# Kernel tuning notes

Hardware: AMD Instinct MI355X
Metric: run time of the kernel (lower is better)

## Reference

```python
import jax, jax.numpy as jnp
import numpy as np
from jax import lax

B, R, F = 100, 15, 4096       # batch, regions, feature dim
V, E, D, A, T = 10000, 1024, 1024, 512, 500  # vocab, embed, decoder, attention, topic
LIN = 1024                    # autoencoder linear output width
NT = 5                        # sentences per paragraph
L = 52                        # max caption length


def setup_inputs() -> dict:
    key = jax.random.key(0)
    ks = jax.random.split(key, 16)
    g = lambda i, shp, s: jax.random.normal(ks[i], shp, jnp.float32) * s
    return {
        "image_features": g(0, (B, R, F), 1.0),
        "encoded_captions": jax.random.randint(ks[1], (B, NT, L), 0, V),
        "caption_lengths": jax.random.randint(ks[2], (B, NT), 1, L),
        # autoencoder
        "W_lt": g(3, (LIN, F), 0.02), "b_lt": jnp.zeros((LIN,), jnp.float32),
        "conv_w": g(4, (6, 1, 15, 26), 0.05), "conv_b": jnp.zeros((6,), jnp.float32),
        # attention MLP (weight_norm linears == plain linears mathematically)
        "W_feat": g(5, (A, F), 0.02), "b_feat": jnp.zeros((A,), jnp.float32),
        "W_dec": g(6, (A, D), 0.02), "b_dec": jnp.zeros((A,), jnp.float32),
        "W_top": g(7, (A, T), 0.02), "b_top": jnp.zeros((A,), jnp.float32),
        "W_full": g(8, (1, A), 0.02), "b_full": jnp.zeros((1,), jnp.float32),
        # embedding + LSTM cells + output heads
        "emb": g(9, (V, E), 0.1),
        "W_ih1": g(10, (4 * D, E + F + D), 0.01), "W_hh1": g(11, (4 * D, D), 0.01),
        "b_ih1": jnp.zeros((4 * D,), jnp.float32), "b_hh1": jnp.zeros((4 * D,), jnp.float32),
        "W_ih2": g(12, (4 * D, F + D), 0.01), "W_hh2": g(13, (4 * D, D), 0.01),
        "b_ih2": jnp.zeros((4 * D,), jnp.float32), "b_hh2": jnp.zeros((4 * D,), jnp.float32),
        "W_fc1": g(14, (V, D), 0.02), "b_fc1": jnp.zeros((V,), jnp.float32),
        "W_fc": g(15, (V, D), 0.02), "b_fc": jnp.zeros((V,), jnp.float32),
    }


def _lstm_cell(x, h, c, W_ih, W_hh, b_ih, b_hh):
    gates = x @ W_ih.T + b_ih + h @ W_hh.T + b_hh
    i, f, g_, o = jnp.split(gates, 4, axis=-1)
    c = jax.nn.sigmoid(f) * c + jax.nn.sigmoid(i) * jnp.tanh(g_)
    h = jax.nn.sigmoid(o) * jnp.tanh(c)
    return h, c


def reference(image_features, encoded_captions, caption_lengths, W_lt, b_lt,
              conv_w, conv_b, W_feat, b_feat, W_dec, b_dec, W_top, b_top,
              W_full, b_full, emb, W_ih1, W_hh1, b_ih1, b_hh1,
              W_ih2, W_hh2, b_ih2, b_hh2, W_fc1, b_fc1, W_fc, b_fc):
    def per_sample(img, caps, lens):
        # img (R,F), caps (NT,L) int, lens (NT,) int
        img_mean = img.mean(0)  # (F,)
        # autoencoder: linear 4096->1024, conv2d(1->6, k=(15,26), stride 2)
        x = (img @ W_lt.T + b_lt)[None, None]  # (1,1,R,LIN)
        conv = lax.conv_general_dilated(x, conv_w, (2, 2), "VALID",
                                        dimension_numbers=("NCHW", "OIHW", "NCHW"))
        topics = conv[0, :, 0, :] + conv_b[:, None]  # (6, T=500)
        att1 = img @ W_feat.T + b_feat               # (R,A), precomputed once
        # last word of each sentence: caps[t, lens[t]-1]
        last_words = jnp.take_along_axis(caps, (lens - 1)[:, None], axis=1)[:, 0]  # (NT,)
        last_embs = emb[last_words]                  # (NT,E)

        def step(carry, tup):
            h1, c1, h2, c2 = carry
            topic_t, emb_t = tup
            # top-down attention LSTM: cat([h2, img_mean, word_emb])
            x1 = jnp.concatenate([h2, img_mean, emb_t])
            h1, c1 = _lstm_cell(x1, h1, c1, W_ih1, W_hh1, b_ih1, b_hh1)
            # attention over R regions (dropout is identity in eval)
            att = jax.nn.relu(att1 + (h1 @ W_dec.T + b_dec) + (topic_t @ W_top.T + b_top))
            scores = att @ W_full[0] + b_full[0]     # (R,)
            alpha = jax.nn.softmax(scores)
            awe = alpha @ img                        # (F,)
            preds1 = h1 @ W_fc1.T + b_fc1            # (V,)
            h2, c2 = _lstm_cell(jnp.concatenate([awe, h1]), h2, c2,
                                W_ih2, W_hh2, b_ih2, b_hh2)
            preds = h2 @ W_fc.T + b_fc               # (V,)
            return (h1, c1, h2, c2), (preds, preds1)

        z = jnp.zeros((D,), img.dtype)
        _, (preds, preds1) = lax.scan(step, (z, z, z, z), (topics[:NT], last_embs))
        return preds, preds1                          # (NT,V) each

    preds, preds1 = jax.vmap(per_sample)(image_features, encoded_captions, caption_lengths)
    return preds, preds1, encoded_captions, caption_lengths - 1
```

## Files before the change

kernel.cpp:

```cpp
#include <hip/hip_runtime.h>

typedef __attribute__((ext_vector_type(8))) short short8;
typedef __attribute__((ext_vector_type(4))) short short4v;
typedef __attribute__((ext_vector_type(4))) float f32x4;

__device__ __forceinline__ unsigned short f2bf(float f) {
  unsigned int u = __float_as_uint(f);
  u += 0x7fffu + ((u >> 16) & 1u);
  return (unsigned short)(u >> 16);
}
__device__ __forceinline__ float bf2f(unsigned short u) {
  return __uint_as_float(((unsigned int)u) << 16);
}
__device__ __forceinline__ float sigm(float x) { return 1.f / (1.f + expf(-x)); }

template<int NKC>
__global__ __launch_bounds__(256) void gemm_v5(
    const unsigned short* __restrict__ X, int ldx,
    const unsigned short* __restrict__ W, int ldw, int N,
    unsigned short* __restrict__ C, long long slotStride)
{
  __shared__ short8 lds[3584];
  const int tid = threadIdx.x;
  const int lane = tid & 63, wv = tid >> 6;
// ... 60 lines not shown
  const int nrow = (ncol < N) ? ncol : (N - 1);
  const long long k0 = (long long)blockIdx.z * (NKC * 256);
  C += (long long)blockIdx.z * slotStride;

  const float* wp = W + (size_t)nrow * ldw + kg + k0;
  const unsigned short* xb = X + (size_t)(mbase + l16) * ldx + kg + k0;
  const size_t xrow = (size_t)16 * ldx;

  f32x4 acc[7];
#pragma unroll
  for (int i = 0; i < 7; ++i) acc[i] = (f32x4){0.f, 0.f, 0.f, 0.f};

  for (int kc = 0; kc < NKC; ++kc) {
    if (kc) __syncthreads();
    float4 wa[8], wb[8];
#pragma unroll
    for (int ks = 0; ks < 8; ++ks) {
      wa[ks] = *(const float4*)(wp + kc * 256 + ks * 32);
      wb[ks] = *(const float4*)(wp + kc * 256 + ks * 32 + 4);
    }
    short8 xst[14];
#pragma unroll
    for (int i = 0; i < 14; ++i) {
      const int f = wv + i * 4, mt = f >> 3, ks = f & 7;
      xst[i] = *(const short8*)(xb + (size_t)mt * xrow + kc * 256 + ks * 32);
    }
#pragma unroll
    for (int i = 0; i < 14; ++i) lds[(wv + i * 4) * 64 + lane] = xst[i];
    __syncthreads();
#pragma unroll
    for (int ks = 0; ks < 8; ++ks) {
      short8 w;
      w[0] = (short)f2bf(wa[ks].x); w[1] = (short)f2bf(wa[ks].y);
      w[2] = (short)f2bf(wa[ks].z); w[3] = (short)f2bf(wa[ks].w);
      w[4] = (short)f2bf(wb[ks].x); w[5] = (short)f2bf(wb[ks].y);
      w[6] = (short)f2bf(wb[ks].z); w[7] = (short)f2bf(wb[ks].w);
#pragma unroll
      for (int mt = 0; mt < 7; ++mt) {
        short8 a = lds[(mt * 8 + ks) * 64 + lane];
        acc[mt] = __builtin_amdgcn_mfma_f32_16x16x32_bf16(a, w, acc[mt], 0, 0, 0);
      }
    }
  }
  if (ncol < N) {
    const int r0 = (lane >> 4) * 4;
#pragma unroll
    for (int mt = 0; mt < 7; ++mt)
#pragma unroll
      for (int r = 0; r < 4; ++r)
        C[(size_t)(mbase + mt * 16 + r0 + r) * N + ncol] = f2bf(acc[mt][r]);
  }
}

__global__ __launch_bounds__(256) void k_pack_all(
    const float* __restrict__ Wih1, const float* __restrict__ Whh1,
    const float* __restrict__ Wih2, const float* __restrict__ Whh2,
    const float* __restrict__ Wfc1, const float* __restrict__ Wdec,
    const float* __restrict__ Wfc,  const float* __restrict__ Wlt,
    const float* __restrict__ Wft,  const float* __restrict__ Wtop,
    unsigned short* __restrict__ Wg1, unsigned short* __restrict__ Wg2,
    unsigned short* __restrict__ Wcat, unsigned short* __restrict__ Wfcb,
    unsigned short* __restrict__ Wltb, unsigned short* __restrict__ Wftb,
    unsigned short* __restrict__ Wtopb)
{
  int i = blockIdx.x * 256 + threadIdx.x;
  float4 v; unsigned short* dst; long long di;
  if (i < 2097152) {
    int row = i >> 9, c4 = i & 511;
    const float* s = (c4 < 256) ? Wih1 + (size_t)row * 6144 + c4 * 4
                                : Whh1 + (size_t)row * 1024 + (c4 - 256) * 4;
    v = *(const float4*)s; dst = Wg1; di = i;
  } else if (i < 8388608) {
    int j = i - 2097152; int row = j / 1536, c4 = j - row * 1536;
    const float* s = (c4 < 1280) ? Wih2 + (size_t)row * 5120 + c4 * 4
                                 : Whh2 + (size_t)row * 1024 + (c4 - 1280) * 4;
    v = *(const float4*)s; dst = Wg2; di = j;
  } else if (i < 11079680) {
    int j = i - 8388608; int row = j >> 8, c4 = j & 255;
    const float* s = (row < 10000) ? Wfc1 + (size_t)row * 1024 + c4 * 4
                                   : Wdec + (size_t)(row - 10000) * 1024 + c4 * 4;
    v = *(const float4*)s; dst = Wcat; di = j;
  } else if (i < 13639680) { int j = i - 11079680; v = ((const float4*)Wfc)[j]; dst = Wfcb; di = j; }
  else if (i < 14688256) { int j = i - 13639680; v = ((const float4*)Wlt)[j]; dst = Wltb; di = j; }
  else if (i < 15212544) { int j = i - 14688256; v = ((const float4*)Wft)[j]; dst = Wftb; di = j; }
  else {
    int j = i - 15212544; int n = j >> 7, c4 = j & 127;
    v = (c4 < 125) ? *(const float4*)(Wtop + (size_t)n * 500 + c4 * 4)
                   : (float4){0.f, 0.f, 0.f, 0.f};
    dst = Wtopb; di = j;
  }
  short4v o; o[0] = (short)f2bf(v.x); o[1] = (short)f2bf(v.y);
  o[2] = (short)f2bf(v.z); o[3] = (short)f2bf(v.w);
  ((short4v*)dst)[di] = o;
}

__global__ __launch_bounds__(256) void k_ximg(const float* __restrict__ src,
                                              unsigned short* __restrict__ dst) {
  int idx = blockIdx.x * 256 + threadIdx.x;
  int row = idx >> 12;
  dst[idx] = (row < 1500) ? f2bf(src[idx]) : (unsigned short)0;
}

__global__ __launch_bounds__(256) void k_mean(const float* __restrict__ img,
                                              unsigned short* __restrict__ dst) {
  int idx = blockIdx.x * 256 + threadIdx.x;
  int b = idx >> 12, f = idx & 4095;
  unsigned short r = 0;
  if (b < 100) {
    float s = 0.f;
    for (int rr = 0; rr < 15; ++rr) s += img[((size_t)b * 15 + rr) * 4096 + f];
    r = f2bf(s * (1.f / 15.f));
  }
  dst[idx] = r;
}

__global__ __launch_bounds__(256) void k_reduce(const unsigned short* __restrict__ P,
    long long ss, int nslots, const float* __restrict__ bias, int colmask,
    float* __restrict__ out, int total) {
  int idx = blockIdx.x * 256 + threadIdx.x;
  if (idx >= total) return;
  float s = bias ? bias[idx & colmask] : 0.f;
  for (int sl = 0; sl < nslots; ++sl) s += bf2f(P[(size_t)sl * ss + idx]);
  out[idx] = s;
}

__global__ __launch_bounds__(512) void k_conv(const unsigned short* __restrict__ px,
    const float* __restrict__ blt, const float* __restrict__ cw,
    const float* __restrict__ cb, float* __restrict__ topics) {
  int b = blockIdx.x;
  __shared__ float L[15 * 1024];
  for (int i = threadIdx.x; i < 15 * 1024; i += 512) {
    float s = blt[i & 1023];
#pragma unroll
    for (int sl = 0; sl < 4; ++sl)
      s += bf2f(px[(size_t)sl * 1605632 + (size_t)b * 15360 + i]);
    L[i] = s;
  }
  __syncthreads();
  for (int idx = threadIdx.x; idx < 2500; idx += 512) {
    int tt = idx / 500, w = idx - tt * 500;
    float s = cb[tt];
    for (int kh = 0; kh < 15; ++kh) {
      const float* lr = &L[kh * 1024 + 2 * w];
      const float* wr = &cw[(tt * 15 + kh) * 26];
#pragma unroll
      for (int kw = 0; kw < 26; ++kw) s += lr[kw] * wr[kw];
    }
    topics[(size_t)b * 2500 + idx] = s;
  }
}

__global__ __launch_bounds__(256) void k_padtop(const float* __restrict__ topics,
    unsigned short* __restrict__ Xtop) {
  int idx = blockIdx.x * 256 + threadIdx.x;
  if (idx >= 560 * 512) return;
  int r = idx >> 9, k = idx & 511;
  Xtop[idx] = (r < 500 && k < 500) ? f2bf(topics[(size_t)r * 500 + k]) : (unsigned short)0;
}

__global__ void k_wc(const int* __restrict__ caps, const int* __restrict__ lens,
                     int* __restrict__ words, float* __restrict__ out2,
                     float* __restrict__ out3) {
  int idx = blockIdx.x * 256 + threadIdx.x;
  if (idx < 26000) out2[idx] = (float)caps[idx];
  if (idx < 500) {
    int len = lens[idx];
    words[idx] = caps[idx * 52 + len - 1];
    out3[idx] = (float)(len - 1);
  }
}

__global__ __launch_bounds__(256) void k_gather(const float* __restrict__ emb,
    const int* __restrict__ words, unsigned short* __restrict__ Xemb) {
  int idx = blockIdx.x * 256 + threadIdx.x;
  int bt = idx >> 10, e = idx & 1023;
  Xemb[idx] = (bt < 500) ? f2bf(emb[(size_t)words[bt] * 1024 + e]) : (unsigned short)0;
}

__global__ __launch_bounds__(256) void k_gbase1(const unsigned short* __restrict__ P,
    const float* __restrict__ bih, const float* __restrict__ bhh,
    float* __restrict__ gb) {
  int idx = blockIdx.x * 256 + threadIdx.x;
  int m = idx >> 12, n = idx & 4095;
  float s = bih[n] + bhh[n];
#pragma unroll
  for (int sl = 0; sl < 8; ++sl) s += bf2f(P[((size_t)sl * 112 + m) * 4096 + n]);
  gb[idx] = s;
}

__global__ __launch_bounds__(256) void k_lstm1(const unsigned short* __restrict__ P,
    const float* __restrict__ gb1, const float* __restrict__ gemb, int t,
    float* __restrict__ c1, unsigned short* __restrict__ Xh1,
    unsigned short* __restrict__ X1, unsigned short* __restrict__ X2) {
  int idx = blockIdx.x * 256 + threadIdx.x;
  int b = idx >> 10, j = idx & 1023;
  float g[4];
#pragma unroll
  for (int x = 0; x < 4; ++x) {
    int col = (x << 10) + j;
    float s = gb1[b * 4096 + col] + gemb[((size_t)b * 5 + t) * 4096 + col];
#pragma unroll
    for (int sl = 0; sl < 8; ++sl) s += bf2f(P[((size_t)sl * 112 + b) * 4096 + col]);
    g[x] = s;
  }
  float c = sigm(g[1]) * c1[idx] + sigm(g[0]) * tanhf(g[2]);
  float h = sigm(g[3]) * tanhf(c);
  c1[idx] = c;
  unsigned short hb = f2bf(h);
  Xh1[idx] = hb;
  X1[b * 2048 + 1024 + j] = hb;
  X2[(size_t)b * 6144 + 4096 + j] = hb;
}

__global__ __launch_bounds__(256) void k_attawe(const float* __restrict__ att1,
    const unsigned short* __restrict__ padec, const float* __restrict__ bdec,
    const float* __restrict__ btop, const unsigned short* __restrict__ ttopb,
    const float* __restrict__ wfull, int t,
    const unsigned short* __restrict__ Ximg, unsigned short* __restrict__ X2) {
  int b = blockIdx.x;
  int tid = threadIdx.x;
  int r = tid & 15, ch = tid >> 4;
  __shared__ float sp[16][17];
  __shared__ float al[16];
  float s = 0.f;
  if (r < 15) {
    const float* a1 = att1 + ((size_t)b * 15 + r) * 512;
    const unsigned short* tp = ttopb + ((size_t)b * 5 + t) * 512;
#pragma unroll
    for (int j = 0; j < 32; ++j) {
      int n = ch * 32 + j;
      float ad = bdec[n] + btop[n]
               + bf2f(padec[((size_t)0 * 112 + b) * 10512 + 10000 + n])
               + bf2f(padec[((size_t)1 * 112 + b) * 10512 + 10000 + n])
               + bf2f(padec[((size_t)2 * 112 + b) * 10512 + 10000 + n])
               + bf2f(padec[((size_t)3 * 112 + b) * 10512 + 10000 + n]);
      float v = a1[n] + ad + bf2f(tp[n]);
      s += fmaxf(v, 0.f) * wfull[n];
    }
  }
  sp[r][ch] = s;
  __syncthreads();
  if (tid == 0) {
    float sc[15];
    float m = -1e30f;
    for (int rr = 0; rr < 15; ++rr) {
      float x = 0.f;
      for (int cc = 0; cc < 16; ++cc) x += sp[rr][cc];
      sc[rr] = x; m = fmaxf(m, x);
    }
    float sum = 0.f;
    for (int rr = 0; rr < 15; ++rr) { sc[rr] = expf(sc[rr] - m); sum += sc[rr]; }
    float inv = 1.f / sum;
    for (int rr = 0; rr < 15; ++rr) al[rr] = sc[rr] * inv;
  }
  __syncthreads();
  for (int f = tid; f < 4096; f += 256) {
    float s2 = 0.f;
#pragma unroll
    for (int rr = 0; rr < 15; ++rr)
      s2 += al[rr] * bf2f(Ximg[((size_t)b * 15 + rr) * 4096 + f]);
    X2[(size_t)b * 6144 + f] = f2bf(s2);
  }
}

__global__ __launch_bounds__(256) void k_lstm2(const unsigned short* __restrict__ P,
    const float* __restrict__ bih, const float* __restrict__ bhh,
    float* __restrict__ c2, unsigned short* __restrict__ Xh2,
    unsigned short* __restrict__ X1, unsigned short* __restrict__ X2) {
  int idx = blockIdx.x * 256 + threadIdx.x;
  int b = idx >> 10, j = idx & 1023;
  float g[4];
#pragma unroll
  for (int x = 0; x < 4; ++x) {
    int col = (x << 10) + j;
    float s = bih[col] + bhh[col];
#pragma unroll
    for (int sl = 0; sl < 12; ++sl) s += bf2f(P[((size_t)sl * 112 + b) * 4096 + col]);
    g[x] = s;
  }
  float c = sigm(g[1]) * c2[idx] + sigm(g[0]) * tanhf(g[2]);
  float h = sigm(g[3]) * tanhf(c);
  c2[idx] = c;
  unsigned short hb = f2bf(h);
  Xh2[idx] = hb;
  X1[b * 2048 + j] = hb;
  X2[(size_t)b * 6144 + 5120 + j] = hb;
}

__global__ __launch_bounds__(256) void k_eppred(const unsigned short* __restrict__ P,
    const float* __restrict__ bias, float* __restrict__ outp, int t, int ldp) {
  int idx = blockIdx.x * 256 + threadIdx.x;
  if (idx >= 1000000) return;
  int b = idx / 10000, v = idx - b * 10000;
  outp[((size_t)b * 5 + t) * 10000 + v] = bias[v]
      + bf2f(P[(size_t)(0 * 112 + b) * ldp + v]) + bf2f(P[(size_t)(112 + b) * ldp + v])
      + bf2f(P[(size_t)(224 + b) * ldp + v])     + bf2f(P[(size_t)(336 + b) * ldp + v]);
}

extern "C" void kernel_launch(void* const* d_in, const int* in_sizes, int n_in,
                              void* d_out, int out_size, void* d_ws, size_t ws_size,
                              hipStream_t stream) {
  (void)in_sizes; (void)n_in; (void)out_size;
  const float* imgf  = (const float*)d_in[0];
  const int*   caps  = (const int*)d_in[1];
  const int*   lens  = (const int*)d_in[2];
  const float* W_lt  = (const float*)d_in[3];
  const float* b_lt  = (const float*)d_in[4];
  const float* convw = (const float*)d_in[5];
  const float* convb = (const float*)d_in[6];
  const float* W_feat = (const float*)d_in[7];
  const float* b_feat = (const float*)d_in[8];
  const float* W_dec = (const float*)d_in[9];
  const float* b_dec = (const float*)d_in[10];
  const float* W_top = (const float*)d_in[11];
  const float* b_top = (const float*)d_in[12];
  const float* W_full = (const float*)d_in[13];
  const float* b_full = (const float*)d_in[14];  (void)b_full;
  const float* emb   = (const float*)d_in[15];
  const float* W_ih1 = (const float*)d_in[16];
  const float* W_hh1 = (const float*)d_in[17];
  const float* b_ih1 = (const float*)d_in[18];
  const float* b_hh1 = (const float*)d_in[19];
  const float* W_ih2 = (const float*)d_in[20];
  const float* W_hh2 = (const float*)d_in[21];
  const float* b_ih2 = (const float*)d_in[22];
  const float* b_hh2 = (const float*)d_in[23];
  const float* W_fc1 = (const float*)d_in[24];
  const float* b_fc1 = (const float*)d_in[25];
  const float* W_fc  = (const float*)d_in[26];
  const float* b_fc  = (const float*)d_in[27];
  float* out = (float*)d_out;

  char* ws = (char*)d_ws;
  size_t off = 0;
  auto alloc = [&](size_t bytes) -> size_t {
    size_t o = off; off = (off + bytes + 255) & ~(size_t)255; return o;
  };
  const size_t oXimg  = alloc(1568ull * 4096 * 2);
  const size_t oXmean = alloc(112ull * 4096 * 2);
  const size_t oXemb  = alloc(560ull * 1024 * 2);
  const size_t oZERO  = off;
  const size_t oX1    = alloc(112ull * 2048 * 2);
  const size_t oX2    = alloc(112ull * 6144 * 2);
  const size_t oXh1   = alloc(112ull * 1024 * 2);
  const size_t oXh2   = alloc(112ull * 1024 * 2);
  const size_t oc1    = alloc(100ull * 1024 * 4);
  const size_t oc2    = alloc(100ull * 1024 * 4);
  const size_t zeroBytes = off - oZERO;
  const size_t otop   = alloc(100ull * 2500 * 4);
  const size_t oXtop  = alloc(560ull * 512 * 2);
  const size_t oTtopb = alloc(560ull * 512 * 2);
  const size_t oatt1  = alloc(1568ull * 512 * 4);
  const size_t ogb1   = alloc(112ull * 4096 * 4);
  const size_t ogemb  = alloc(560ull * 4096 * 4);
  const size_t owords = alloc(512ull * 4);
  const size_t opg    = alloc(12ull * 112 * 4096 * 2);
  const size_t opx    = alloc(4ull * 560 * 4096 * 2);
  const size_t oWg1   = alloc(4096ull * 2048 * 2);
  const size_t oWg2   = alloc(4096ull * 6144 * 2);
  const size_t oWcat  = alloc(10512ull * 1024 * 2);
  const size_t oWfcb  = alloc(10000ull * 1024 * 2);
  const size_t oWltb  = alloc(1024ull * 4096 * 2);
  const size_t oWftb  = alloc(512ull * 4096 * 2);
  const size_t oWtopb = alloc(512ull * 512 * 2);
  if (ws_size < off) return;

  unsigned short* Ximg  = (unsigned short*)(ws + oXimg);
  unsigned short* Xmean = (unsigned short*)(ws + oXmean);
  unsigned short* Xemb  = (unsigned short*)(ws + oXemb);
  unsigned short* X1    = (unsigned short*)(ws + oX1);
  unsigned short* X2    = (unsigned short*)(ws + oX2);
  unsigned short* Xh1   = (unsigned short*)(ws + oXh1);
  unsigned short* Xh2   = (unsigned short*)(ws + oXh2);
  float* c1    = (float*)(ws + oc1);
  float* c2    = (float*)(ws + oc2);
  float* topics = (float*)(ws + otop);
  unsigned short* Xtop  = (unsigned short*)(ws + oXtop);
  unsigned short* Ttopb = (unsigned short*)(ws + oTtopb);
  float* att1  = (float*)(ws + oatt1);
  float* gb1   = (float*)(ws + ogb1);
  float* gemb  = (float*)(ws + ogemb);
  int*   words = (int*)(ws + owords);
  unsigned short* pg = (unsigned short*)(ws + opg);
  unsigned short* px = (unsigned short*)(ws + opx);
  unsigned short* Wg1   = (unsigned short*)(ws + oWg1);
  unsigned short* Wg2   = (unsigned short*)(ws + oWg2);
  unsigned short* Wcat  = (unsigned short*)(ws + oWcat);
  unsigned short* Wfcb  = (unsigned short*)(ws + oWfcb);
  unsigned short* Wltb  = (unsigned short*)(ws + oWltb);
  unsigned short* Wftb  = (unsigned short*)(ws + oWftb);
  unsigned short* Wtopb = (unsigned short*)(ws + oWtopb);

  const long long S4  = 112ll * 4096;
  const long long SP1 = 112ll * 10512;
  const long long SP  = 112ll * 10000;

  hipMemsetAsync(ws + oZERO, 0, zeroBytes, stream);

  k_ximg<<<25088, 256, 0, stream>>>(imgf, Ximg);
  k_mean<<<1792, 256, 0, stream>>>(imgf, Xmean);
  k_pack_all<<<59680, 256, 0, stream>>>(W_ih1, W_hh1, W_ih2, W_hh2, W_fc1, W_dec,
                                        W_fc, W_lt, W_feat, W_top,
                                        Wg1, Wg2, Wcat, Wfcb, Wltb, Wftb, Wtopb);
  gemm_v5<4><<<dim3(16, 14, 4), 256, 0, stream>>>(Ximg, 4096, Wltb, 4096, 1024,
                                                  px, 1568ll * 1024);
  k_conv<<<100, 512, 0, stream>>>(px, b_lt, convw, convb, topics);
  k_padtop<<<1120, 256, 0, stream>>>(topics, Xtop);
  gemm_v5<2><<<dim3(8, 5, 1), 256, 0, stream>>>(Xtop, 512, Wtopb, 512, 512, Ttopb, 0);
  gemm_v5<4><<<dim3(8, 14, 4), 256, 0, stream>>>(Ximg, 4096, Wftb, 4096, 512,
                                                 px, 1568ll * 512);
  k_reduce<<<3136, 256, 0, stream>>>(px, 1568ll * 512, 4, b_feat, 511, att1, 1568 * 512);
  k_wc<<<102, 256, 0, stream>>>(caps, lens, words, out + 10000000, out + 10026000);
  k_gather<<<2240, 256, 0, stream>>>(emb, words, Xemb);
  gemm_v5f<2><<<dim3(64, 1, 8), 256, 0, stream>>>(Xmean, 4096, W_ih1 + 1024, 6144, 4096,
                                                  pg, S4);
  k_gbase1<<<1792, 256, 0, stream>>>(pg, b_ih1, b_hh1, gb1);
  gemm_v5f<1><<<dim3(64, 5, 4), 256, 0, stream>>>(Xemb, 1024, W_ih1 + 5120, 6144, 4096,
                                                  px, 560ll * 4096);
  k_reduce<<<8960, 256, 0, stream>>>(px, 560ll * 4096, 4, nullptr, 4095, gemb, 560 * 4096);

  for (int t = 0; t < 5; ++t) {
    gemm_v5<1><<<dim3(64, 1, 8), 256, 0, stream>>>(X1, 2048, Wg1, 2048, 4096, pg, S4);
    k_lstm1<<<400, 256, 0, stream>>>(pg, gb1, gemb, t, c1, Xh1, X1, X2);
    gemm_v5<1><<<dim3(165, 1, 4), 256, 0, stream>>>(Xh1, 1024, Wcat, 1024, 10512, px, SP1);
    k_attawe<<<100, 256, 0, stream>>>(att1, px, b_dec, b_top, Ttopb, W_full, t, Ximg, X2);
    k_eppred<<<3907, 256, 0, stream>>>(px, b_fc1, out + 5000000, t, 10512);
    gemm_v5<2><<<dim3(64, 1, 12), 256, 0, stream>>>(X2, 6144, Wg2, 6144, 4096, pg, S4);
    k_lstm2<<<400, 256, 0, stream>>>(pg, b_ih2, b_hh2, c2, Xh2, X1, X2);
    gemm_v5<1><<<dim3(157, 1, 4), 256, 0, stream>>>(Xh2, 1024, Wfcb, 1024, 10000, px, SP);
    k_eppred<<<3907, 256, 0, stream>>>(px, b_fc, out, t, 10000);
  }
}
```

Baseline: 704.5 us.

## Fuse bias/reduction into fp32-weight GEMMs and drop split-K partial buffers

Adds GEMM variants that read fp32 weights directly, convert to bf16 in registers, and write fp32 output with bias applied, removing the split-K partial buffers and the separate reduce/epilogue kernels for the autoencoder linear, feature projection, embedding gates and both vocab heads. Packing of the large fc/fc1/dec/lt/feat weights is removed, image conversion and mean are merged into one kernel, and split-K for the LSTM gate GEMMs is halved. This cuts launches and partial-sum traffic, but fewer K-splits mean fewer blocks per GEMM and longer serial K loops, which can lower parallelism on the small-M recurrent GEMMs.

```diff
diff --git a/kernel.cpp b/kernel.cpp
--- a/kernel.cpp
+++ b/kernel.cpp
@@ -136,15 +136,151 @@
   }
 }
 
+template<int NKC>
+__global__ __launch_bounds__(256) void gemm_dwf(
+    const unsigned short* __restrict__ X, int ldx,
+    const float* __restrict__ W, int ldw, int N,
+    float* __restrict__ outF, const float* __restrict__ bias,
+    long long ldc, int rowLim)
+{
+  __shared__ short8 lds[3584];
+  const int tid = threadIdx.x;
+  const int lane = tid & 63, wv = tid >> 6;
+  const int l16 = lane & 15, kg = (lane >> 4) * 8;
+  const int mbase = blockIdx.y * 112;
+  const int ncol = blockIdx.x * 64 + wv * 16 + l16;
+  const int nrow = (ncol < N) ? ncol : (N - 1);
+
+  const float* wp = W + (size_t)nrow * ldw + kg;
+  const unsigned short* xb = X + (size_t)(mbase + l16) * ldx + kg;
+  const size_t xrow = (size_t)16 * ldx;
+
+  f32x4 acc[7];
+#pragma unroll
+  for (int i = 0; i < 7; ++i) acc[i] = (f32x4){0.f, 0.f, 0.f, 0.f};
+
+  for (int kc = 0; kc < NKC; ++kc) {
+    if (kc) __syncthreads();
+    float4 wa[8], wb[8];
+#pragma unroll
+    for (int ks = 0; ks < 8; ++ks) {
+      wa[ks] = *(const float4*)(wp + kc * 256 + ks * 32);
+      wb[ks] = *(const float4*)(wp + kc * 256 + ks * 32 + 4);
+    }
+    short8 xst[14];
+#pragma unroll
+    for (int i = 0; i < 14; ++i) {
+      const int f = wv + i * 4, mt = f >> 3, ks = f & 7;
+      xst[i] = *(const short8*)(xb + (size_t)mt * xrow + kc * 256 + ks * 32);
+    }
+#pragma unroll
+    for (int i = 0; i < 14; ++i) lds[(wv + i * 4) * 64 + lane] = xst[i];
+    __syncthreads();
+#pragma unroll
+    for (int ks = 0; ks < 8; ++ks) {
+      short8 w;
+      w[0] = (short)f2bf(wa[ks].x); w[1] = (short)f2bf(wa[ks].y);
+      w[2] = (short)f2bf(wa[ks].z); w[3] = (short)f2bf(wa[ks].w);
+      w[4] = (short)f2bf(wb[ks].x); w[5] = (short)f2bf(wb[ks].y);
+      w[6] = (short)f2bf(wb[ks].z); w[7] = (short)f2bf(wb[ks].w);
+#pragma unroll
+      for (int mt = 0; mt < 7; ++mt) {
+        short8 a = lds[(mt * 8 + ks) * 64 + lane];
+        acc[mt] = __builtin_amdgcn_mfma_f32_16x16x32_bf16(a, w, acc[mt], 0, 0, 0);
+      }
+    }
+  }
+  if (ncol < N) {
+    const float bv = bias ? bias[ncol] : 0.f;
+    const int r0 = (lane >> 4) * 4;
+#pragma unroll
+    for (int mt = 0; mt < 7; ++mt)
+#pragma unroll
+      for (int r = 0; r < 4; ++r) {
+        const int row = mbase + mt * 16 + r0 + r;
+        if (row < rowLim) outF[(size_t)row * ldc + ncol] = acc[mt][r] + bv;
+      }
+  }
+}
+
+template<int NKC>
+__global__ __launch_bounds__(256) void gemm_dwf_split(
+    const unsigned short* __restrict__ X, int ldx,
+    const float* __restrict__ W1, const float* __restrict__ W2,
+    float* __restrict__ outF, const float* __restrict__ bias,
+    unsigned short* __restrict__ aux)
+{
+  __shared__ short8 lds[3584];
+  const int tid = threadIdx.x;
+  const int lane = tid & 63, wv = tid >> 6;
+  const int l16 = lane & 15, kg = (lane >> 4) * 8;
+  const int ncol0 = blockIdx.x * 64 + wv * 16 + l16;
+  const int ncol = (ncol0 < 10512) ? ncol0 : 10511;
+  const float* wp = ((ncol < 10000) ? W1 + (size_t)ncol * 1024
+                                    : W2 + (size_t)(ncol - 10000) * 1024) + kg;
+  const unsigned short* xb = X + (size_t)l16 * ldx + kg;
+  const size_t xrow = (size_t)16 * ldx;
+
+  f32x4 acc[7];
+#pragma unroll
+  for (int i = 0; i < 7; ++i) acc[i] = (f32x4){0.f, 0.f, 0.f, 0.f};
+
+  for (int kc = 0; kc < NKC; ++kc) {
+    if (kc) __syncthreads();
+    float4 wa[8], wb[8];
+#pragma unroll
+    for (int ks = 0; ks < 8; ++ks) {
+      wa[ks] = *(const float4*)(wp + kc * 256 + ks * 32);
+      wb[ks] = *(const float4*)(wp + kc * 256 + ks * 32 + 4);
+    }
+    short8 xst[14];
+#pragma unroll
+    for (int i = 0; i < 14; ++i) {
+      const int f = wv + i * 4, mt = f >> 3, ks = f & 7;
+      xst[i] = *(const short8*)(xb + (size_t)mt * xrow + kc * 256 + ks * 32);
+    }
+#pragma unroll
+    for (int i = 0; i < 14; ++i) lds[(wv + i * 4) * 64 + lane] = xst[i];
+    __syncthreads();
+#pragma unroll
+    for (int ks = 0; ks < 8; ++ks) {
+      short8 w;
+      w[0] = (short)f2bf(wa[ks].x); w[1] = (short)f2bf(wa[ks].y);
+      w[2] = (short)f2bf(wa[ks].z); w[3] = (short)f2bf(wa[ks].w);
+      w[4] = (short)f2bf(wb[ks].x); w[5] = (short)f2bf(wb[ks].y);
+      w[6] = (short)f2bf(wb[ks].z); w[7] = (short)f2bf(wb[ks].w);
+#pragma unroll
+      for (int mt = 0; mt < 7; ++mt) {
+        short8 a = lds[(mt * 8 + ks) * 64 + lane];
+        acc[mt] = __builtin_amdgcn_mfma_f32_16x16x32_bf16(a, w, acc[mt], 0, 0, 0);
+      }
+    }
+  }
+  if (ncol0 < 10000) {
+    const float bv = bias[ncol0];
+    const int r0 = (lane >> 4) * 4;
+#pragma unroll
+    for (int mt = 0; mt < 7; ++mt)
+#pragma unroll
+      for (int r = 0; r < 4; ++r) {
+        const int row = mt * 16 + r0 + r;
+        if (row < 100) outF[(size_t)row * 50000 + ncol0] = acc[mt][r] + bv;
+      }
+  } else if (ncol0 < 10512) {
+    const int r0 = (lane >> 4) * 4;
+#pragma unroll
+    for (int mt = 0; mt < 7; ++mt)
+#pragma unroll
+      for (int r = 0; r < 4; ++r)
+        aux[(size_t)(mt * 16 + r0 + r) * 512 + (ncol0 - 10000)] = f2bf(acc[mt][r]);
+  }
+}
+
 __global__ __launch_bounds__(256) void k_pack_all(
     const float* __restrict__ Wih1, const float* __restrict__ Whh1,
     const float* __restrict__ Wih2, const float* __restrict__ Whh2,
-    const float* __restrict__ Wfc1, const float* __restrict__ Wdec,
-    const float* __restrict__ Wfc,  const float* __restrict__ Wlt,
-    const float* __restrict__ Wft,  const float* __restrict__ Wtop,
+    const float* __restrict__ Wtop,
     unsigned short* __restrict__ Wg1, unsigned short* __restrict__ Wg2,
-    unsigned short* __restrict__ Wcat, unsigned short* __restrict__ Wfcb,
-    unsigned short* __restrict__ Wltb, unsigned short* __restrict__ Wftb,
     unsigned short* __restrict__ Wtopb)
 {
   int i = blockIdx.x * 256 + threadIdx.x;
@@ -159,16 +295,9 @@
     const float* s = (c4 < 1280) ? Wih2 + (size_t)row * 5120 + c4 * 4
                                  : Whh2 + (size_t)row * 1024 + (c4 - 1280) * 4;
     v = *(const float4*)s; dst = Wg2; di = j;
-  } else if (i < 11079680) {
-    int j = i - 8388608; int row = j >> 8, c4 = j & 255;
-    const float* s = (row < 10000) ? Wfc1 + (size_t)row * 1024 + c4 * 4
-                                   : Wdec + (size_t)(row - 10000) * 1024 + c4 * 4;
-    v = *(const float4*)s; dst = Wcat; di = j;
-  } else if (i < 13639680) { int j = i - 11079680; v = ((const float4*)Wfc)[j]; dst = Wfcb; di = j; }
-  else if (i < 14688256) { int j = i - 13639680; v = ((const float4*)Wlt)[j]; dst = Wltb; di = j; }
-  else if (i < 15212544) { int j = i - 14688256; v = ((const float4*)Wft)[j]; dst = Wftb; di = j; }
-  else {
-    int j = i - 15212544; int n = j >> 7, c4 = j & 127;
+  } else {
+    int j = i - 8388608; if (j >= 65536) return;
+    int n = j >> 7, c4 = j & 127;
     v = (c4 < 125) ? *(const float4*)(Wtop + (size_t)n * 500 + c4 * 4)
                    : (float4){0.f, 0.f, 0.f, 0.f};
     dst = Wtopb; di = j;
@@ -178,48 +307,26 @@
   ((short4v*)dst)[di] = o;
 }
 
-__global__ __launch_bounds__(256) void k_ximg(const float* __restrict__ src,
-                                              unsigned short* __restrict__ dst) {
-  int idx = blockIdx.x * 256 + threadIdx.x;
-  int row = idx >> 12;
-  dst[idx] = (row < 1500) ? f2bf(src[idx]) : (unsigned short)0;
-}
-
-__global__ __launch_bounds__(256) void k_mean(const float* __restrict__ img,
-                                              unsigned short* __restrict__ dst) {
+__global__ __launch_bounds__(256) void k_ximg2(const float* __restrict__ img,
+    unsigned short* __restrict__ Ximg, unsigned short* __restrict__ Xmean) {
   int idx = blockIdx.x * 256 + threadIdx.x;
   int b = idx >> 12, f = idx & 4095;
-  unsigned short r = 0;
-  if (b < 100) {
-    float s = 0.f;
-    for (int rr = 0; rr < 15; ++rr) s += img[((size_t)b * 15 + rr) * 4096 + f];
-    r = f2bf(s * (1.f / 15.f));
-  }
-  dst[idx] = r;
-}
-
-__global__ __launch_bounds__(256) void k_reduce(const unsigned short* __restrict__ P,
-    long long ss, int nslots, const float* __restrict__ bias, int colmask,
-    float* __restrict__ out, int total) {
-  int idx = blockIdx.x * 256 + threadIdx.x;
-  if (idx >= total) return;
-  float s = bias ? bias[idx & colmask] : 0.f;
-  for (int sl = 0; sl < nslots; ++sl) s += bf2f(P[(size_t)sl * ss + idx]);
-  out[idx] = s;
-}
-
-__global__ __launch_bounds__(512) void k_conv(const unsigned short* __restrict__ px,
-    const float* __restrict__ blt, const float* __restrict__ cw,
-    const float* __restrict__ cb, float* __restrict__ topics) {
+  float s = 0.f;
+#pragma unroll
+  for (int r = 0; r < 15; ++r) {
+    float v = img[((size_t)(b * 15 + r) << 12) + f];
+    s += v;
+    Ximg[((size_t)(b * 15 + r) << 12) + f] = f2bf(v);
+  }
+  Xmean[((size_t)b << 12) + f] = f2bf(s * (1.f / 15.f));
+}
+
+__global__ __launch_bounds__(512) void k_conv(const float* __restrict__ lin,
+    const float* __restrict__ cw, const float* __restrict__ cb,
+    float* __restrict__ topics) {
   int b = blockIdx.x;
   __shared__ float L[15 * 1024];
-  for (int i = threadIdx.x; i < 15 * 1024; i += 512) {
-    float s = blt[i & 1023];
-#pragma unroll
-    for (int sl = 0; sl < 4; ++sl)
-      s += bf2f(px[(size_t)sl * 1605632 + (size_t)b * 15360 + i]);
-    L[i] = s;
-  }
+  for (int i = threadIdx.x; i < 15 * 1024; i += 512) L[i] = lin[(size_t)b * 15360 + i];
   __syncthreads();
   for (int idx = threadIdx.x; idx < 2500; idx += 512) {
     int tt = idx / 500, w = idx - tt * 500;
@@ -268,7 +375,7 @@
   int m = idx >> 12, n = idx & 4095;
   float s = bih[n] + bhh[n];
 #pragma unroll
-  for (int sl = 0; sl < 8; ++sl) s += bf2f(P[((size_t)sl * 112 + m) * 4096 + n]);
+  for (int sl = 0; sl < 4; ++sl) s += bf2f(P[((size_t)sl * 112 + m) * 4096 + n]);
   gb[idx] = s;
 }
 
@@ -284,7 +391,7 @@
     int col = (x << 10) + j;
     float s = gb1[b * 4096 + col] + gemb[((size_t)b * 5 + t) * 4096 + col];
 #pragma unroll
-    for (int sl = 0; sl < 8; ++sl) s += bf2f(P[((size_t)sl * 112 + b) * 4096 + col]);
+    for (int sl = 0; sl < 4; ++sl) s += bf2f(P[((size_t)sl * 112 + b) * 4096 + col]);
     g[x] = s;
   }
   float c = sigm(g[1]) * c1[idx] + sigm(g[0]) * tanhf(g[2]);
@@ -313,11 +420,7 @@
 #pragma unroll
     for (int j = 0; j < 32; ++j) {
       int n = ch * 32 + j;
-      float ad = bdec[n] + btop[n]
-               + bf2f(padec[((size_t)0 * 112 + b) * 10512 + 10000 + n])
-               + bf2f(padec[((size_t)1 * 112 + b) * 10512 + 10000 + n])
-               + bf2f(padec[((size_t)2 * 112 + b) * 10512 + 10000 + n])
-               + bf2f(padec[((size_t)3 * 112 + b) * 10512 + 10000 + n]);
+      float ad = bdec[n] + btop[n] + bf2f(padec[(size_t)b * 512 + n]);
       float v = a1[n] + ad + bf2f(tp[n]);
       s += fmaxf(v, 0.f) * wfull[n];
     }
@@ -359,7 +462,7 @@
     int col = (x << 10) + j;
     float s = bih[col] + bhh[col];
 #pragma unroll
-    for (int sl = 0; sl < 12; ++sl) s += bf2f(P[((size_t)sl * 112 + b) * 4096 + col]);
+    for (int sl = 0; sl < 6; ++sl) s += bf2f(P[((size_t)sl * 112 + b) * 4096 + col]);
     g[x] = s;
   }
   float c = sigm(g[1]) * c2[idx] + sigm(g[0]) * tanhf(g[2]);
@@ -369,16 +472,6 @@
   Xh2[idx] = hb;
   X1[b * 2048 + j] = hb;
   X2[(size_t)b * 6144 + 5120 + j] = hb;
-}
-
-__global__ __launch_bounds__(256) void k_eppred(const unsigned short* __restrict__ P,
-    const float* __restrict__ bias, float* __restrict__ outp, int t, int ldp) {
-  int idx = blockIdx.x * 256 + threadIdx.x;
-  if (idx >= 1000000) return;
-  int b = idx / 10000, v = idx - b * 10000;
-  outp[((size_t)b * 5 + t) * 10000 + v] = bias[v]
-      + bf2f(P[(size_t)(0 * 112 + b) * ldp + v]) + bf2f(P[(size_t)(112 + b) * ldp + v])
-      + bf2f(P[(size_t)(224 + b) * ldp + v])     + bf2f(P[(size_t)(336 + b) * ldp + v]);
 }
 
 extern "C" void kernel_launch(void* const* d_in, const int* in_sizes, int n_in,
@@ -420,10 +513,9 @@
   auto alloc = [&](size_t bytes) -> size_t {
     size_t o = off; off = (off + bytes + 255) & ~(size_t)255; return o;
   };
+  const size_t oZERO  = off;
   const size_t oXimg  = alloc(1568ull * 4096 * 2);
   const size_t oXmean = alloc(112ull * 4096 * 2);
-  const size_t oXemb  = alloc(560ull * 1024 * 2);
-  const size_t oZERO  = off;
   const size_t oX1    = alloc(112ull * 2048 * 2);
   const size_t oX2    = alloc(112ull * 6144 * 2);
   const size_t oXh1   = alloc(112ull * 1024 * 2);
@@ -431,6 +523,8 @@
   const size_t oc1    = alloc(100ull * 1024 * 4);
   const size_t oc2    = alloc(100ull * 1024 * 4);
   const size_t zeroBytes = off - oZERO;
+  const size_t oXemb  = alloc(560ull * 1024 * 2);
+  const size_t olin   = alloc(1568ull * 1024 * 4);
   const size_t otop   = alloc(100ull * 2500 * 4);
   const size_t oXtop  = alloc(560ull * 512 * 2);
   const size_t oTtopb = alloc(560ull * 512 * 2);
@@ -438,14 +532,10 @@
   const size_t ogb1   = alloc(112ull * 4096 * 4);
   const size_t ogemb  = alloc(560ull * 4096 * 4);
   const size_t owords = alloc(512ull * 4);
-  const size_t opg    = alloc(12ull * 112 * 4096 * 2);
-  const size_t opx    = alloc(4ull * 560 * 4096 * 2);
+  const size_t opg    = alloc(6ull * 112 * 4096 * 2);
+  const size_t opadec = alloc(112ull * 512 * 2);
   const size_t oWg1   = alloc(4096ull * 2048 * 2);
   const size_t oWg2   = alloc(4096ull * 6144 * 2);
-  const size_t oWcat  = alloc(10512ull * 1024 * 2);
-  const size_t oWfcb  = alloc(10000ull * 1024 * 2);
-  const size_t oWltb  = alloc(1024ull * 4096 * 2);
-  const size_t oWftb  = alloc(512ull * 4096 * 2);
   const size_t oWtopb = alloc(512ull * 512 * 2);
   if (ws_size < off) return;
 
@@ -458,6 +548,7 @@
   unsigned short* Xh2   = (unsigned short*)(ws + oXh2);
   float* c1    = (float*)(ws + oc1);
   float* c2    = (float*)(ws + oc2);
+  float* lin   = (float*)(ws + olin);
   float* topics = (float*)(ws + otop);
   unsigned short* Xtop  = (unsigned short*)(ws + oXtop);
   unsigned short* Ttopb = (unsigned short*)(ws + oTtopb);
@@ -465,53 +556,44 @@
   float* gb1   = (float*)(ws + ogb1);
   float* gemb  = (float*)(ws + ogemb);
   int*   words = (int*)(ws + owords);
-  unsigned short* pg = (unsigned short*)(ws + opg);
-  unsigned short* px = (unsigned short*)(ws + opx);
+  unsigned short* pg    = (unsigned short*)(ws + opg);
+  unsigned short* padec = (unsigned short*)(ws + opadec);
   unsigned short* Wg1   = (unsigned short*)(ws + oWg1);
   unsigned short* Wg2   = (unsigned short*)(ws + oWg2);
-  unsigned short* Wcat  = (unsigned short*)(ws + oWcat);
-  unsigned short* Wfcb  = (unsigned short*)(ws + oWfcb);
-  unsigned short* Wltb  = (unsigned short*)(ws + oWltb);
-  unsigned short* Wftb  = (unsigned short*)(ws + oWftb);
   unsigned short* Wtopb = (unsigned short*)(ws + oWtopb);
 
-  const long long S4  = 112ll * 4096;
-  const long long SP1 = 112ll * 10512;
-  const long long SP  = 112ll * 10000;
+  const long long S4 = 112ll * 4096;
 
   hipMemsetAsync(ws + oZERO, 0, zeroBytes, stream);
 
-  k_ximg<<<25088, 256, 0, stream>>>(imgf, Ximg);
-  k_mean<<<1792, 256, 0, stream>>>(imgf, Xmean);
-  k_pack_all<<<59680, 256, 0, stream>>>(W_ih1, W_hh1, W_ih2, W_hh2, W_fc1, W_dec,
-                                        W_fc, W_lt, W_feat, W_top,
-                                        Wg1, Wg2, Wcat, Wfcb, Wltb, Wftb, Wtopb);
-  gemm_v5<4><<<dim3(16, 14, 4), 256, 0, stream>>>(Ximg, 4096, Wltb, 4096, 1024,
-                                                  px, 1568ll * 1024);
-  k_conv<<<100, 512, 0, stream>>>(px, b_lt, convw, convb, topics);
+  k_ximg2<<<1600, 256, 0, stream>>>(imgf, Ximg, Xmean);
+  k_pack_all<<<33024, 256, 0, stream>>>(W_ih1, W_hh1, W_ih2, W_hh2, W_top,
+                                        Wg1, Wg2, Wtopb);
+  gemm_dwf<16><<<dim3(16, 14, 1), 256, 0, stream>>>(Ximg, 4096, W_lt, 4096, 1024,
+                                                    lin, b_lt, 1024, 1568);
+  k_conv<<<100, 512, 0, stream>>>(lin, convw, convb, topics);
   k_padtop<<<1120, 256, 0, stream>>>(topics, Xtop);
   gemm_v5<2><<<dim3(8, 5, 1), 256, 0, stream>>>(Xtop, 512, Wtopb, 512, 512, Ttopb, 0);
-  gemm_v5<4><<<dim3(8, 14, 4), 256, 0, stream>>>(Ximg, 4096, Wftb, 4096, 512,
-                                                 px, 1568ll * 512);
-  k_reduce<<<3136, 256, 0, stream>>>(px, 1568ll * 512, 4, b_feat, 511, att1, 1568 * 512);
+  gemm_dwf<16><<<dim3(8, 14, 1), 256, 0, stream>>>(Ximg, 4096, W_feat, 4096, 512,
+                                                   att1, b_feat, 512, 1568);
   k_wc<<<102, 256, 0, stream>>>(caps, lens, words, out + 10000000, out + 10026000);
   k_gather<<<2240, 256, 0, stream>>>(emb, words, Xemb);
-  gemm_v5f<2><<<dim3(64, 1, 8), 256, 0, stream>>>(Xmean, 4096, W_ih1 + 1024, 6144, 4096,
+  gemm_v5f<4><<<dim3(64, 1, 4), 256, 0, stream>>>(Xmean, 4096, W_ih1 + 1024, 6144, 4096,
                                                   pg, S4);
   k_gbase1<<<1792, 256, 0, stream>>>(pg, b_ih1, b_hh1, gb1);
-  gemm_v5f<1><<<dim3(64, 5, 4), 256, 0, stream>>>(Xemb, 1024, W_ih1 + 5120, 6144, 4096,
-                                                  px, 560ll * 4096);
-  k_reduce<<<8960, 256, 0, stream>>>(px, 560ll * 4096, 4, nullptr, 4095, gemb, 560 * 4096);
+  gemm_dwf<4><<<dim3(64, 5, 1), 256, 0, stream>>>(Xemb, 1024, W_ih1 + 5120, 6144, 4096,
+                                                  gemb, nullptr, 4096, 560);
 
   for (int t = 0; t < 5; ++t) {
-    gemm_v5<1><<<dim3(64, 1, 8), 256, 0, stream>>>(X1, 2048, Wg1, 2048, 4096, pg, S4);
+    gemm_v5<2><<<dim3(64, 1, 4), 256, 0, stream>>>(X1, 2048, Wg1, 2048, 4096, pg, S4);
     k_lstm1<<<400, 256, 0, stream>>>(pg, gb1, gemb, t, c1, Xh1, X1, X2);
-    gemm_v5<1><<<dim3(165, 1, 4), 256, 0, stream>>>(Xh1, 1024, Wcat, 1024, 10512, px, SP1);
-    k_attawe<<<100, 256, 0, stream>>>(att1, px, b_dec, b_top, Ttopb, W_full, t, Ximg, X2);
-    k_eppred<<<3907, 256, 0, stream>>>(px, b_fc1, out + 5000000, t, 10512);
-    gemm_v5<2><<<dim3(64, 1, 12), 256, 0, stream>>>(X2, 6144, Wg2, 6144, 4096, pg, S4);
+    gemm_dwf_split<4><<<dim3(165, 1, 1), 256, 0, stream>>>(
+        Xh1, 1024, W_fc1, W_dec, out + 5000000 + t * 10000, b_fc1, padec);
+    k_attawe<<<100, 256, 0, stream>>>(att1, padec, b_dec, b_top, Ttopb, W_full, t,
+                                      Ximg, X2);
+    gemm_v5<4><<<dim3(64, 1, 6), 256, 0, stream>>>(X2, 6144, Wg2, 6144, 4096, pg, S4);
     k_lstm2<<<400, 256, 0, stream>>>(pg, b_ih2, b_hh2, c2, Xh2, X1, X2);
-    gemm_v5<1><<<dim3(157, 1, 4), 256, 0, stream>>>(Xh2, 1024, Wfcb, 1024, 10000, px, SP);
-    k_eppred<<<3907, 256, 0, stream>>>(px, b_fc, out, t, 10000);
-  }
-}
+    gemm_dwf<4><<<dim3(157, 1, 1), 256, 0, stream>>>(Xh2, 1024, W_fc, 1024, 10000,
+                                                     out + t * 10000, b_fc, 50000, 100);
+  }
+}
```

After: 789.2 us. 1.12x slower.

## Fuse preprocessing kernels and read fp32 weights directly in image GEMMs

Applied to the files above, without the earlier changes.

Several small kernels are merged: bf16 image conversion with the region mean, conv with topic padding/bf16 packing, word lookup with embedding gather, and the attention step with the fc1 prediction epilogue. The W_lt and W_feat GEMMs now use the fp32-weight GEMM variant with split-K 8 instead of pre-packing those weights to bf16, which drops part of the pack kernel. This cuts launches and intermediate round trips, in exchange for more split-K partial sums to reduce and a larger scratch buffer. Xtop is now zeroed by the memset so that its padding stays correct.

```diff
diff --git a/kernel.cpp b/kernel.cpp
--- a/kernel.cpp
+++ b/kernel.cpp
@@ -140,11 +140,9 @@
     const float* __restrict__ Wih1, const float* __restrict__ Whh1,
     const float* __restrict__ Wih2, const float* __restrict__ Whh2,
     const float* __restrict__ Wfc1, const float* __restrict__ Wdec,
-    const float* __restrict__ Wfc,  const float* __restrict__ Wlt,
-    const float* __restrict__ Wft,  const float* __restrict__ Wtop,
+    const float* __restrict__ Wfc,  const float* __restrict__ Wtop,
     unsigned short* __restrict__ Wg1, unsigned short* __restrict__ Wg2,
     unsigned short* __restrict__ Wcat, unsigned short* __restrict__ Wfcb,
-    unsigned short* __restrict__ Wltb, unsigned short* __restrict__ Wftb,
     unsigned short* __restrict__ Wtopb)
 {
   int i = blockIdx.x * 256 + threadIdx.x;
@@ -165,10 +163,9 @@
                                    : Wdec + (size_t)(row - 10000) * 1024 + c4 * 4;
     v = *(const float4*)s; dst = Wcat; di = j;
   } else if (i < 13639680) { int j = i - 11079680; v = ((const float4*)Wfc)[j]; dst = Wfcb; di = j; }
-  else if (i < 14688256) { int j = i - 13639680; v = ((const float4*)Wlt)[j]; dst = Wltb; di = j; }
-  else if (i < 15212544) { int j = i - 14688256; v = ((const float4*)Wft)[j]; dst = Wftb; di = j; }
   else {
-    int j = i - 15212544; int n = j >> 7, c4 = j & 127;
+    int j = i - 13639680; if (j >= 65536) return;
+    int n = j >> 7, c4 = j & 127;
     v = (c4 < 125) ? *(const float4*)(Wtop + (size_t)n * 500 + c4 * 4)
                    : (float4){0.f, 0.f, 0.f, 0.f};
     dst = Wtopb; di = j;
@@ -178,24 +175,18 @@
   ((short4v*)dst)[di] = o;
 }
 
-__global__ __launch_bounds__(256) void k_ximg(const float* __restrict__ src,
-                                              unsigned short* __restrict__ dst) {
-  int idx = blockIdx.x * 256 + threadIdx.x;
-  int row = idx >> 12;
-  dst[idx] = (row < 1500) ? f2bf(src[idx]) : (unsigned short)0;
-}
-
-__global__ __launch_bounds__(256) void k_mean(const float* __restrict__ img,
-                                              unsigned short* __restrict__ dst) {
+__global__ __launch_bounds__(256) void k_ximg2(const float* __restrict__ img,
+    unsigned short* __restrict__ Ximg, unsigned short* __restrict__ Xmean) {
   int idx = blockIdx.x * 256 + threadIdx.x;
   int b = idx >> 12, f = idx & 4095;
-  unsigned short r = 0;
-  if (b < 100) {
-    float s = 0.f;
-    for (int rr = 0; rr < 15; ++rr) s += img[((size_t)b * 15 + rr) * 4096 + f];
-    r = f2bf(s * (1.f / 15.f));
-  }
-  dst[idx] = r;
+  float s = 0.f;
+#pragma unroll
+  for (int r = 0; r < 15; ++r) {
+    float v = img[((size_t)(b * 15 + r) << 12) + f];
+    s += v;
+    Ximg[((size_t)(b * 15 + r) << 12) + f] = f2bf(v);
+  }
+  Xmean[((size_t)b << 12) + f] = f2bf(s * (1.f / 15.f));
 }
 
 __global__ __launch_bounds__(256) void k_reduce(const unsigned short* __restrict__ P,
@@ -210,13 +201,13 @@
 
 __global__ __launch_bounds__(512) void k_conv(const unsigned short* __restrict__ px,
     const float* __restrict__ blt, const float* __restrict__ cw,
-    const float* __restrict__ cb, float* __restrict__ topics) {
+    const float* __restrict__ cb, unsigned short* __restrict__ Xtop) {
   int b = blockIdx.x;
   __shared__ float L[15 * 1024];
   for (int i = threadIdx.x; i < 15 * 1024; i += 512) {
     float s = blt[i & 1023];
 #pragma unroll
-    for (int sl = 0; sl < 4; ++sl)
+    for (int sl = 0; sl < 8; ++sl)
       s += bf2f(px[(size_t)sl * 1605632 + (size_t)b * 15360 + i]);
     L[i] = s;
   }
@@ -230,35 +221,22 @@
 #pragma unroll
       for (int kw = 0; kw < 26; ++kw) s += lr[kw] * wr[kw];
     }
-    topics[(size_t)b * 2500 + idx] = s;
-  }
-}
-
-__global__ __launch_bounds__(256) void k_padtop(const float* __restrict__ topics,
-    unsigned short* __restrict__ Xtop) {
-  int idx = blockIdx.x * 256 + threadIdx.x;
-  if (idx >= 560 * 512) return;
-  int r = idx >> 9, k = idx & 511;
-  Xtop[idx] = (r < 500 && k < 500) ? f2bf(topics[(size_t)r * 500 + k]) : (unsigned short)0;
-}
-
-__global__ void k_wc(const int* __restrict__ caps, const int* __restrict__ lens,
-                     int* __restrict__ words, float* __restrict__ out2,
-                     float* __restrict__ out3) {
-  int idx = blockIdx.x * 256 + threadIdx.x;
+    Xtop[((size_t)(b * 5 + tt)) * 512 + w] = f2bf(s);
+  }
+}
+
+__global__ __launch_bounds__(256) void k_gw(const int* __restrict__ caps,
+    const int* __restrict__ lens, const float* __restrict__ emb,
+    unsigned short* __restrict__ Xemb, float* __restrict__ out2,
+    float* __restrict__ out3) {
+  int idx = blockIdx.x * 256 + threadIdx.x;
+  int bt = idx >> 10, e = idx & 1023;
+  if (bt < 500) {
+    int w = caps[bt * 52 + lens[bt] - 1];
+    Xemb[idx] = f2bf(emb[(size_t)w * 1024 + e]);
+  } else if (bt < 560) Xemb[idx] = 0;
   if (idx < 26000) out2[idx] = (float)caps[idx];
-  if (idx < 500) {
-    int len = lens[idx];
-    words[idx] = caps[idx * 52 + len - 1];
-    out3[idx] = (float)(len - 1);
-  }
-}
-
-__global__ __launch_bounds__(256) void k_gather(const float* __restrict__ emb,
-    const int* __restrict__ words, unsigned short* __restrict__ Xemb) {
-  int idx = blockIdx.x * 256 + threadIdx.x;
-  int bt = idx >> 10, e = idx & 1023;
-  Xemb[idx] = (bt < 500) ? f2bf(emb[(size_t)words[bt] * 1024 + e]) : (unsigned short)0;
+  if (idx < 500) out3[idx] = (float)(lens[idx] - 1);
 }
 
 __global__ __launch_bounds__(256) void k_gbase1(const unsigned short* __restrict__ P,
@@ -296,11 +274,21 @@
   X2[(size_t)b * 6144 + 4096 + j] = hb;
 }
 
-__global__ __launch_bounds__(256) void k_attawe(const float* __restrict__ att1,
-    const unsigned short* __restrict__ padec, const float* __restrict__ bdec,
+__global__ __launch_bounds__(256) void k_attpred(const float* __restrict__ att1,
+    const unsigned short* __restrict__ px, const float* __restrict__ bdec,
     const float* __restrict__ btop, const unsigned short* __restrict__ ttopb,
     const float* __restrict__ wfull, int t,
-    const unsigned short* __restrict__ Ximg, unsigned short* __restrict__ X2) {
+    const unsigned short* __restrict__ Ximg, unsigned short* __restrict__ X2,
+    const float* __restrict__ bfc1, float* __restrict__ outp) {
+  if (blockIdx.x >= 100) {
+    int idx = (blockIdx.x - 100) * 256 + threadIdx.x;
+    if (idx >= 1000000) return;
+    int b = idx / 10000, v = idx - b * 10000;
+    outp[((size_t)b * 5 + t) * 10000 + v] = bfc1[v]
+        + bf2f(px[(size_t)b * 10512 + v])         + bf2f(px[(size_t)(112 + b) * 10512 + v])
+        + bf2f(px[(size_t)(224 + b) * 10512 + v]) + bf2f(px[(size_t)(336 + b) * 10512 + v]);
+    return;
+  }
   int b = blockIdx.x;
   int tid = threadIdx.x;
   int r = tid & 15, ch = tid >> 4;
@@ -314,10 +302,10 @@
     for (int j = 0; j < 32; ++j) {
       int n = ch * 32 + j;
       float ad = bdec[n] + btop[n]
-               + bf2f(padec[((size_t)0 * 112 + b) * 10512 + 10000 + n])
-               + bf2f(padec[((size_t)1 * 112 + b) * 10512 + 10000 + n])
-               + bf2f(padec[((size_t)2 * 112 + b) * 10512 + 10000 + n])
-               + bf2f(padec[((size_t)3 * 112 + b) * 10512 + 10000 + n]);
+               + bf2f(px[((size_t)0 * 112 + b) * 10512 + 10000 + n])
+               + bf2f(px[((size_t)1 * 112 + b) * 10512 + 10000 + n])
+               + bf2f(px[((size_t)2 * 112 + b) * 10512 + 10000 + n])
+               + bf2f(px[((size_t)3 * 112 + b) * 10512 + 10000 + n]);
       float v = a1[n] + ad + bf2f(tp[n]);
       s += fmaxf(v, 0.f) * wfull[n];
     }
@@ -377,8 +365,8 @@
   if (idx >= 1000000) return;
   int b = idx / 10000, v = idx - b * 10000;
   outp[((size_t)b * 5 + t) * 10000 + v] = bias[v]
-      + bf2f(P[(size_t)(0 * 112 + b) * ldp + v]) + bf2f(P[(size_t)(112 + b) * ldp + v])
-      + bf2f(P[(size_t)(224 + b) * ldp + v])     + bf2f(P[(size_t)(336 + b) * ldp + v]);
+      + bf2f(P[(size_t)b * ldp + v])         + bf2f(P[(size_t)(112 + b) * ldp + v])
+      + bf2f(P[(size_t)(224 + b) * ldp + v]) + bf2f(P[(size_t)(336 + b) * ldp + v]);
 }
 
 extern "C" void kernel_launch(void* const* d_in, const int* in_sizes, int n_in,
@@ -420,32 +408,28 @@
   auto alloc = [&](size_t bytes) -> size_t {
     size_t o = off; off = (off + bytes + 255) & ~(size_t)255; return o;
   };
+  const size_t oZERO  = off;
   const size_t oXimg  = alloc(1568ull * 4096 * 2);
   const size_t oXmean = alloc(112ull * 4096 * 2);
-  const size_t oXemb  = alloc(560ull * 1024 * 2);
-  const size_t oZERO  = off;
   const size_t oX1    = alloc(112ull * 2048 * 2);
   const size_t oX2    = alloc(112ull * 6144 * 2);
   const size_t oXh1   = alloc(112ull * 1024 * 2);
   const size_t oXh2   = alloc(112ull * 1024 * 2);
   const size_t oc1    = alloc(100ull * 1024 * 4);
   const size_t oc2    = alloc(100ull * 1024 * 4);
+  const size_t oXtop  = alloc(560ull * 512 * 2);
   const size_t zeroBytes = off - oZERO;
-  const size_t otop   = alloc(100ull * 2500 * 4);
-  const size_t oXtop  = alloc(560ull * 512 * 2);
+  const size_t oXemb  = alloc(560ull * 1024 * 2);
   const size_t oTtopb = alloc(560ull * 512 * 2);
   const size_t oatt1  = alloc(1568ull * 512 * 4);
   const size_t ogb1   = alloc(112ull * 4096 * 4);
   const size_t ogemb  = alloc(560ull * 4096 * 4);
-  const size_t owords = alloc(512ull * 4);
   const size_t opg    = alloc(12ull * 112 * 4096 * 2);
-  const size_t opx    = alloc(4ull * 560 * 4096 * 2);
+  const size_t opx    = alloc(8ull * 1568 * 1024 * 2);
   const size_t oWg1   = alloc(4096ull * 2048 * 2);
   const size_t oWg2   = alloc(4096ull * 6144 * 2);
   const size_t oWcat  = alloc(10512ull * 1024 * 2);
   const size_t oWfcb  = alloc(10000ull * 1024 * 2);
-  const size_t oWltb  = alloc(1024ull * 4096 * 2);
-  const size_t oWftb  = alloc(512ull * 4096 * 2);
   const size_t oWtopb = alloc(512ull * 512 * 2);
   if (ws_size < off) return;
 
@@ -458,21 +442,17 @@
   unsigned short* Xh2   = (unsigned short*)(ws + oXh2);
   float* c1    = (float*)(ws + oc1);
   float* c2    = (float*)(ws + oc2);
-  float* topics = (float*)(ws + otop);
   unsigned short* Xtop  = (unsigned short*)(ws + oXtop);
   unsigned short* Ttopb = (unsigned short*)(ws + oTtopb);
   float* att1  = (float*)(ws + oatt1);
   float* gb1   = (float*)(ws + ogb1);
   float* gemb  = (float*)(ws + ogemb);
-  int*   words = (int*)(ws + owords);
-  unsigned short* pg = (unsigned short*)(ws + opg);
-  unsigned short* px = (unsigned short*)(ws + opx);
+  unsigned short* pg    = (unsigned short*)(ws + opg);
+  unsigned short* px    = (unsigned short*)(ws + opx);
   unsigned short* Wg1   = (unsigned short*)(ws + oWg1);
   unsigned short* Wg2   = (unsigned short*)(ws + oWg2);
   unsigned short* Wcat  = (unsigned short*)(ws + oWcat);
   unsigned short* Wfcb  = (unsigned short*)(ws + oWfcb);
-  unsigned short* Wltb  = (unsigned short*)(ws + oWltb);
-  unsigned short* Wftb  = (unsigned short*)(ws + oWftb);
   unsigned short* Wtopb = (unsigned short*)(ws + oWtopb);
 
   const long long S4  = 112ll * 4096;
@@ -481,21 +461,17 @@
 
   hipMemsetAsync(ws + oZERO, 0, zeroBytes, stream);
 
-  k_ximg<<<25088, 256, 0, stream>>>(imgf, Ximg);
-  k_mean<<<1792, 256, 0, stream>>>(imgf, Xmean);
-  k_pack_all<<<59680, 256, 0, stream>>>(W_ih1, W_hh1, W_ih2, W_hh2, W_fc1, W_dec,
-                                        W_fc, W_lt, W_feat, W_top,
-                                        Wg1, Wg2, Wcat, Wfcb, Wltb, Wftb, Wtopb);
-  gemm_v5<4><<<dim3(16, 14, 4), 256, 0, stream>>>(Ximg, 4096, Wltb, 4096, 1024,
-                                                  px, 1568ll * 1024);
-  k_conv<<<100, 512, 0, stream>>>(px, b_lt, convw, convb, topics);
-  k_padtop<<<1120, 256, 0, stream>>>(topics, Xtop);
+  k_ximg2<<<1600, 256, 0, stream>>>(imgf, Ximg, Xmean);
+  k_pack_all<<<53536, 256, 0, stream>>>(W_ih1, W_hh1, W_ih2, W_hh2, W_fc1, W_dec,
+                                        W_fc, W_top, Wg1, Wg2, Wcat, Wfcb, Wtopb);
+  gemm_v5f<2><<<dim3(16, 14, 8), 256, 0, stream>>>(Ximg, 4096, W_lt, 4096, 1024,
+                                                   px, 1568ll * 1024);
+  k_conv<<<100, 512, 0, stream>>>(px, b_lt, convw, convb, Xtop);
   gemm_v5<2><<<dim3(8, 5, 1), 256, 0, stream>>>(Xtop, 512, Wtopb, 512, 512, Ttopb, 0);
-  gemm_v5<4><<<dim3(8, 14, 4), 256, 0, stream>>>(Ximg, 4096, Wftb, 4096, 512,
-                                                 px, 1568ll * 512);
-  k_reduce<<<3136, 256, 0, stream>>>(px, 1568ll * 512, 4, b_feat, 511, att1, 1568 * 512);
-  k_wc<<<102, 256, 0, stream>>>(caps, lens, words, out + 10000000, out + 10026000);
-  k_gather<<<2240, 256, 0, stream>>>(emb, words, Xemb);
+  gemm_v5f<2><<<dim3(8, 14, 8), 256, 0, stream>>>(Ximg, 4096, W_feat, 4096, 512,
+                                                  px, 1568ll * 512);
+  k_reduce<<<3136, 256, 0, stream>>>(px, 1568ll * 512, 8, b_feat, 511, att1, 1568 * 512);
+  k_gw<<<2240, 256, 0, stream>>>(caps, lens, emb, Xemb, out + 10000000, out + 10026000);
   gemm_v5f<2><<<dim3(64, 1, 8), 256, 0, stream>>>(Xmean, 4096, W_ih1 + 1024, 6144, 4096,
                                                   pg, S4);
   k_gbase1<<<1792, 256, 0, stream>>>(pg, b_ih1, b_hh1, gb1);
@@ -507,8 +483,8 @@
     gemm_v5<1><<<dim3(64, 1, 8), 256, 0, stream>>>(X1, 2048, Wg1, 2048, 4096, pg, S4);
     k_lstm1<<<400, 256, 0, stream>>>(pg, gb1, gemb, t, c1, Xh1, X1, X2);
     gemm_v5<1><<<dim3(165, 1, 4), 256, 0, stream>>>(Xh1, 1024, Wcat, 1024, 10512, px, SP1);
-    k_attawe<<<100, 256, 0, stream>>>(att1, px, b_dec, b_top, Ttopb, W_full, t, Ximg, X2);
-    k_eppred<<<3907, 256, 0, stream>>>(px, b_fc1, out + 5000000, t, 10512);
+    k_attpred<<<4007, 256, 0, stream>>>(att1, px, b_dec, b_top, Ttopb, W_full, t,
+                                        Ximg, X2, b_fc1, out + 5000000);
     gemm_v5<2><<<dim3(64, 1, 12), 256, 0, stream>>>(X2, 6144, Wg2, 6144, 4096, pg, S4);
     k_lstm2<<<400, 256, 0, stream>>>(pg, b_ih2, b_hh2, c2, Xh2, X1, X2);
     gemm_v5<1><<<dim3(157, 1, 4), 256, 0, stream>>>(Xh2, 1024, Wfcb, 1024, 10000, px, SP);
```

Measured after the change: 688.6 us. 1.02x faster.
